# Performance work log

Hardware: AMD Instinct MI355X
Metric: run time of the kernel (lower is better)

## Reference

```python
import jax, jax.numpy as jnp
import numpy as np

N, K, D, H = 20000, 32, 256, 8
HD = D // H
DFF = 4 * D
EPS = 1e-5


def _layernorm(x, gamma, beta):
    mu = jnp.mean(x, axis=-1, keepdims=True)
    var = jnp.mean(jnp.square(x - mu), axis=-1, keepdims=True)
    return (x - mu) * jax.lax.rsqrt(var + EPS) * gamma + beta


def setup_inputs() -> dict:
    key = jax.random.key(0)
    ks = jax.random.split(key, 16)
    s = 0.02
    return {
        "x": jax.random.normal(ks[0], (N, D), jnp.float32),
        "attention_samples": jax.random.randint(ks[1], (N, K), 0, N),
        "Wq": jax.random.normal(ks[2], (D, D), jnp.float32) * s,
        "bq": jnp.zeros((D,), jnp.float32),
        "Wk": jax.random.normal(ks[3], (D, D), jnp.float32) * s,
        "bk": jnp.zeros((D,), jnp.float32),
        "Wv": jax.random.normal(ks[4], (D, D), jnp.float32) * s,
        "bv": jnp.zeros((D,), jnp.float32),
        "Wo": jax.random.normal(ks[5], (D, D), jnp.float32) * s,
        "bo": jnp.zeros((D,), jnp.float32),
        "W1": jax.random.normal(ks[6], (D, DFF), jnp.float32) * s,
        "b1": jnp.zeros((DFF,), jnp.float32),
        "W2": jax.random.normal(ks[7], (DFF, D), jnp.float32) * s,
        "b2": jnp.zeros((D,), jnp.float32),
        "g1": jnp.ones((D,), jnp.float32),
        "be1": jnp.zeros((D,), jnp.float32),
        "g2": jnp.ones((D,), jnp.float32),
        "be2": jnp.zeros((D,), jnp.float32),
    }


def reference(x, attention_samples, Wq, bq, Wk, bk, Wv, bv, Wo, bo,
              W1, b1, W2, b2, g1, be1, g2, be2):
    # --- per-node MHA: query = node itself, keys/values = k sampled neighbors ---
    q = (x @ Wq + bq).reshape(N, H, HD)                    # [N,H,hd]
    g = x[attention_samples]                               # [N,K,D] gathered neighbors
    kk = (g @ Wk + bk).reshape(N, K, H, HD)                # [N,K,H,hd]
    vv = (g @ Wv + bv).reshape(N, K, H, HD)
    scale = 1.0 / jnp.sqrt(jnp.asarray(HD, x.dtype))
    scores = jnp.einsum("nhd,nkhd->nhk", q, kk) * scale    # [N,H,K]
    attn = jax.nn.softmax(scores, axis=-1)
    o = jnp.einsum("nhk,nkhd->nhd", attn, vv).reshape(N, D)
    attn_out = o @ Wo + bo                                 # out_proj
    x = _layernorm(x + attn_out, g1, be1)
    # --- FFN ---
    ff = jax.nn.relu(x @ W1 + b1) @ W2 + b2
    x = _layernorm(x + ff, g2, be2)
    return x
```

## Files before the change

kernel.cpp:

```cpp
#include <hip/hip_runtime.h>

#define NN 20000
#define KNEI 32
#define DIM 256
#define NHEAD 8
#define HDIM 32
#define DFFN 1024
#define QKVD 768

typedef __attribute__((ext_vector_type(8))) __bf16 bf16x8;
typedef __attribute__((ext_vector_type(8))) unsigned short u16x8;
typedef __attribute__((ext_vector_type(4))) unsigned short u16x4;
typedef __attribute__((ext_vector_type(4))) float f32x4;
typedef __attribute__((ext_vector_type(2))) float f32x2;

static __device__ __forceinline__ float b2f(unsigned short u) {
    return __builtin_bit_cast(float, (unsigned)u << 16);
}
static __device__ __forceinline__ float blo(unsigned w) {
    return __builtin_bit_cast(float, w << 16);
}
static __device__ __forceinline__ float bhi(unsigned w) {
    return __builtin_bit_cast(float, w & 0xffff0000u);
}
static __device__ __forceinline__ unsigned short f2b(float f) {
    unsigned u = __builtin_bit_cast(unsigned, f);
    return (unsigned short)((u + 0x7fff + ((u >> 16) & 1)) >> 16);
}

static __device__ __forceinline__ unsigned char fp8enc(float v) {
#if defined(__HIP_DEVICE_COMPILE__) && __has_builtin(__builtin_amdgcn_cvt_pk_fp8_f32)
    return (unsigned char)(__builtin_amdgcn_cvt_pk_fp8_f32(v, v, 0u, false) & 0xffu);
#else
    unsigned u = __builtin_bit_cast(unsigned, v);
    unsigned s = u >> 31;
    unsigned a = u & 0x7fffffffu;
    if (a >= 0x43e00000u) return (unsigned char)((s << 7) | 0x7e);
    float af = __builtin_bit_cast(float, a);
    if (af < 0.015625f) {
        unsigned r = (unsigned)(af * 512.0f + 0.5f);
        if (r >= 8u) return (unsigned char)((s << 7) | 0x08);
        return (unsigned char)((s << 7) | r);
    }
    unsigned lsb = (a >> 20) & 1u;
    a += 0x7ffffu + lsb;
    unsigned e = (a >> 23) - 120u;
    unsigned m = (a >> 20) & 7u;
    unsigned code = (e << 3) | m;
    if (code > 0x7eu) code = 0x7eu;
    return (unsigned char)((s << 7) | code);
#endif
}

template<int SEL>
static __device__ __forceinline__ float fp8dec(unsigned word) {
#if defined(__HIP_DEVICE_COMPILE__) && __has_builtin(__builtin_amdgcn_cvt_f32_fp8)
    return __builtin_amdgcn_cvt_f32_fp8(word, SEL);
#else
    unsigned b = (word >> (SEL * 8)) & 0xffu;
    unsigned s = (b >> 7) & 1u;
    unsigned e = (b >> 3) & 0xfu;
    unsigned m = b & 7u;
    float v;
    if (e == 0) v = (float)m * 0.001953125f;
    else        v = __builtin_bit_cast(float, ((e + 120u) << 23) | (m << 20));
    return s ? -v : v;
#endif
}

template<bool HI>
static __device__ __forceinline__ f32x2 fp8pk(unsigned word) {
#if defined(__HIP_DEVICE_COMPILE__) && __has_builtin(__builtin_amdgcn_cvt_pk_f32_fp8)
    return __builtin_amdgcn_cvt_pk_f32_fp8((int)word, HI);
#else
    f32x2 r;
    r.x = fp8dec<HI ? 2 : 0>(word);
    r.y = fp8dec<HI ? 3 : 1>(word);
    return r;
#endif
}

#define GLD16(src, dst)                                                          \
    __builtin_amdgcn_global_load_lds(                                            \
        (const __attribute__((address_space(1))) void*)(const void*)(src),       \
        (__attribute__((address_space(3))) void*)(void*)(dst), 16, 0, 0)

template<int BM, int RELU, int WF32, int WBF16, int SPLIT>
__global__ __launch_bounds__(256) void gemm_mfma(const unsigned short* __restrict__ A,
                                                 const unsigned short* __restrict__ Bt,
                                                 const float* __restrict__ bias,
                                                 float* __restrict__ Cf,
                                                 unsigned short* __restrict__ Cb,
                                                 unsigned char* __restrict__ kvb,
                                                 int M, int N, int K)
{
    constexpr int BN = 128, BK = 32;
    constexpr int MI = BM / 32;
    constexpr int NI = BN / 32;

    __shared__ unsigned short As[BM * BK];
    __shared__ unsigned short Bs[BN * BK];

    const int tid  = threadIdx.x;
    const int wid  = tid >> 6;
    const int lane = tid & 63;
    const int bm = blockIdx.x * BM;
    const int bn = blockIdx.y * BN;
    const int wr = (wid >> 1) * (BM / 2);
    const int wc = (wid & 1) * (BN / 2);
    const int r0   = lane & 15;
    const int kblk = (lane >> 4) * 8;

    f32x4 acc[MI][NI];
    #pragma unroll
    for (int i = 0; i < MI; ++i)
        #pragma unroll
        for (int j = 0; j < NI; ++j)
            acc[i][j] = (f32x4){0.f, 0.f, 0.f, 0.f};

    for (int k0 = 0; k0 < K; k0 += BK) {
        constexpr int ACH = BM * 4;
        #pragma unroll
        for (int t = 0; t < ACH / 256; ++t) {
            int c = t * 256 + tid;
            int row = bm + (c >> 2);
            if (row >= M) row = M - 1;
            GLD16(A + (size_t)row * K + k0 + (c & 3) * 8,
                  &As[(t * 256 + wid * 64) * 8]);
        }
        #pragma unroll
        for (int t = 0; t < (BN * 4) / 256; ++t) {
            int c = t * 256 + tid;
            GLD16(Bt + (size_t)(bn + (c >> 2)) * K + k0 + (c & 3) * 8,
                  &Bs[(t * 256 + wid * 64) * 8]);
        }
        __syncthreads();

        bf16x8 af[MI], bfr[NI];
        #pragma unroll
        for (int mi = 0; mi < MI; ++mi)
            af[mi] = __builtin_bit_cast(bf16x8,
                     *(const u16x8*)&As[(wr + mi * 16 + r0) * BK + kblk]);
        #pragma unroll
        for (int ni = 0; ni < NI; ++ni)
            bfr[ni] = __builtin_bit_cast(bf16x8,
                     *(const u16x8*)&Bs[(wc + ni * 16 + r0) * BK + kblk]);
        #pragma unroll
        for (int mi = 0; mi < MI; ++mi)
            #pragma unroll
            for (int ni = 0; ni < NI; ++ni)
                acc[mi][ni] = __builtin_amdgcn_mfma_f32_16x16x32_bf16(
                    af[mi], bfr[ni], acc[mi][ni], 0, 0, 0);
        __syncthreads();
    }

    const int r4 = (lane >> 4) * 4;
    #pragma unroll
    for (int mi = 0; mi < MI; ++mi)
        #pragma unroll
        for (int ni = 0; ni < NI; ++ni) {
            const int col = bn + wc + ni * 16 + r0;
            const float bb = bias[col];
            #pragma unroll
            for (int r = 0; r < 4; ++r) {
                const int row = bm + wr + mi * 16 + r4 + r;
                if (row < M) {
                    float v = acc[mi][ni][r] + bb;
                    if (RELU) v = fmaxf(v, 0.f);
                    if (SPLIT) {
                        if (col < 256) Cb[(size_t)row * DIM + col] = f2b(v);
                        else kvb[(size_t)row * 512 + (col - 256)] = fp8enc(v);
                    } else {
                        if (WF32)  Cf[(size_t)row * N + col] = v;
                        if (WBF16) Cb[(size_t)row * N + col] = f2b(v);
                    }
                }
            }
        }
}

__global__ __launch_bounds__(256) void attn_f8(const unsigned short* __restrict__ q,
                                               const unsigned char* __restrict__ kv,
                                               const int* __restrict__ samp,
                                               unsigned short* __restrict__ o)
{
    const int n = blockIdx.x;
    const int tid = threadIdx.x;
    const int wid = tid >> 6;
    const int lane = tid & 63;
    const int j = lane & 31;
    const int hs = lane >> 5;
    const int h = wid * 2 + hs;

    const int kidx = samp[n * KNEI + j];

    const uint4* qp = (const uint4*)(q + (size_t)n * DIM + h * HDIM);
    const uint4 qa = qp[0], qb = qp[1], qc = qp[2], qd = qp[3];
    const unsigned qw[16] = {qa.x, qa.y, qa.z, qa.w, qb.x, qb.y, qb.z, qb.w,
                             qc.x, qc.y, qc.z, qc.w, qd.x, qd.y, qd.z, qd.w};

    const unsigned char* krow = kv + (size_t)kidx * 512 + h * HDIM;
    const uint4 k0 = *(const uint4*)krow;
    const uint4 k1 = *(const uint4*)(krow + 16);
    const unsigned kw[8] = {k0.x, k0.y, k0.z, k0.w, k1.x, k1.y, k1.z, k1.w};

    float s = 0.f;
    #pragma unroll
    for (int i = 0; i < 8; ++i) {
        f32x2 ka = fp8pk<false>(kw[i]);
        f32x2 kb = fp8pk<true>(kw[i]);
        unsigned q0 = qw[2 * i], q1 = qw[2 * i + 1];
        s = fmaf(blo(q0), ka.x, s);
        s = fmaf(bhi(q0), ka.y, s);
        s = fmaf(blo(q1), kb.x, s);
        s = fmaf(bhi(q1), kb.y, s);
    }
    s *= 0.17677669529663687f;

    float m = s;
    #pragma unroll
    for (int sh = 16; sh; sh >>= 1) m = fmaxf(m, __shfl_xor(m, sh));
    float e = __expf(s - m);
    float sum = e;
    #pragma unroll
    for (int sh = 16; sh; sh >>= 1) sum += __shfl_xor(sum, sh);
    const float p = __fdividef(e, sum);

    const int d = j;
    const int pbits = __builtin_bit_cast(int, p);
    const int pbase = hs * 128;
    const int voff = 256 + h * HDIM + d;
    float acc = 0.f;
    #pragma unroll
    for (int jj = 0; jj < KNEI; ++jj) {
        const int kj = __builtin_amdgcn_readlane(kidx, jj);
        const float pj = __builtin_bit_cast(float,
            __builtin_amdgcn_ds_bpermute(pbase + jj * 4, pbits));
        const unsigned char* vp = kv + (size_t)kj * 512 + voff;
        acc = fmaf(pj, fp8dec<0>((unsigned)*vp), acc);
    }
    o[(size_t)n * DIM + h * HDIM + d] = f2b(acc);
}

template<int XF32, int WFOUT>
__global__ __launch_bounds__(256) void add_ln(const float* __restrict__ xf,
                                              const unsigned short* __restrict__ xb,
                                              const unsigned short* __restrict__ y,
                                              const float* __restrict__ gamma,
                                              const float* __restrict__ beta,
                                              float* __restrict__ outf,
                                              unsigned short* __restrict__ outb, int M)
{
    const int row = blockIdx.x * 4 + (threadIdx.x >> 6);
    const int lane = threadIdx.x & 63;
    if (row >= M) return;

    float s0, s1, s2, s3;
    if (XF32) {
        const float4 xv = *(const float4*)(xf + (size_t)row * DIM + lane * 4);
        s0 = xv.x; s1 = xv.y; s2 = xv.z; s3 = xv.w;
    } else {
        const u16x4 xv = *(const u16x4*)(xb + (size_t)row * DIM + lane * 4);
        s0 = b2f(xv[0]); s1 = b2f(xv[1]); s2 = b2f(xv[2]); s3 = b2f(xv[3]);
    }
    const u16x4 yv = *(const u16x4*)(y + (size_t)row * DIM + lane * 4);
    s0 += b2f(yv[0]); s1 += b2f(yv[1]); s2 += b2f(yv[2]); s3 += b2f(yv[3]);

    float sum = s0 + s1 + s2 + s3;
    float sq = s0 * s0 + s1 * s1 + s2 * s2 + s3 * s3;
    #pragma unroll
    for (int sh = 32; sh; sh >>= 1) {
        sum += __shfl_xor(sum, sh);
        sq  += __shfl_xor(sq, sh);
    }
    float mean = sum * (1.f / 256.f);
    float var = sq * (1.f / 256.f) - mean * mean;
    float rstd = rsqrtf(var + 1e-5f);

    const float4 gv = *(const float4*)(gamma + lane * 4);
    const float4 bv = *(const float4*)(beta + lane * 4);
    float o0 = (s0 - mean) * rstd * gv.x + bv.x;
    float o1 = (s1 - mean) * rstd * gv.y + bv.y;
    float o2 = (s2 - mean) * rstd * gv.z + bv.z;
    float o3 = (s3 - mean) * rstd * gv.w + bv.w;
    if (WFOUT) {
        float4 ov = { o0, o1, o2, o3 };
        *(float4*)(outf + (size_t)row * DIM + lane * 4) = ov;
    } else {
        u16x4 bb = { f2b(o0), f2b(o1), f2b(o2), f2b(o3) };
        *(u16x4*)(outb + (size_t)row * DIM + lane * 4) = bb;
    }
}

__global__ __launch_bounds__(256) void cvt_bf16(const float* __restrict__ in,
                                                unsigned short* __restrict__ out, int n4)
{
    int i = blockIdx.x * 256 + threadIdx.x;
    if (i < n4) {
        float4 v = ((const float4*)in)[i];
        u16x4 b = { f2b(v.x), f2b(v.y), f2b(v.z), f2b(v.w) };
        ((u16x4*)out)[i] = b;
    }
}

__global__ __launch_bounds__(256) void cvt_transpose(const float* __restrict__ W,
                                                     unsigned short* __restrict__ Wt,
                                                     int K, int N)
{
    __shared__ float t[32][33];
    const int n0 = blockIdx.x * 32, k0 = blockIdx.y * 32;
    const int tx = threadIdx.x & 31, ty = threadIdx.x >> 5;
    #pragma unroll
    for (int i = 0; i < 32; i += 8)
        t[ty + i][tx] = W[(size_t)(k0 + ty + i) * N + n0 + tx];
    __syncthreads();
    #pragma unroll
    for (int i = 0; i < 32; i += 8)
        Wt[(size_t)(n0 + ty + i) * K + k0 + tx] = f2b(t[tx][ty + i]);
}

__global__ __launch_bounds__(256) void cvt_transpose4(const float* __restrict__ Wa,
                                                      const float* __restrict__ Wb,
                                                      const float* __restrict__ Wc,
                                                      const float* __restrict__ Wd,
                                                      unsigned short* __restrict__ Ta,
                                                      unsigned short* __restrict__ Tb,
                                                      unsigned short* __restrict__ Tc,
                                                      unsigned short* __restrict__ Td)
{
    const float* W; unsigned short* T;
    switch (blockIdx.z) {
        case 0:  W = Wa; T = Ta; break;
        case 1:  W = Wb; T = Tb; break;
        case 2:  W = Wc; T = Tc; break;
        default: W = Wd; T = Td; break;
    }
    __shared__ float t[32][33];
    const int n0 = blockIdx.x * 32, k0 = blockIdx.y * 32;
    const int tx = threadIdx.x & 31, ty = threadIdx.x >> 5;
    #pragma unroll
    for (int i = 0; i < 32; i += 8)
        t[ty + i][tx] = W[(size_t)(k0 + ty + i) * DIM + n0 + tx];
    __syncthreads();
    #pragma unroll
    for (int i = 0; i < 32; i += 8)
        T[(size_t)(n0 + ty + i) * DIM + k0 + tx] = f2b(t[tx][ty + i]);
}

__global__ void concat_bias(const float* a, const float* b, const float* c, float* out)
{
    int i = blockIdx.x * 256 + threadIdx.x;
    if (i < 256) out[i] = a[i];
    else if (i < 512) out[i] = b[i - 256];
    else if (i < 768) out[i] = c[i - 512];
}

extern "C" void kernel_launch(void* const* d_in, const int* in_sizes, int n_in,
                              void* d_out, int out_size, void* d_ws, size_t ws_size,
                              hipStream_t stream)
{
    const float* x    = (const float*)d_in[0];
    const int*   samp = (const int*)  d_in[1];
    const float* Wq = (const float*)d_in[2];  const float* bq = (const float*)d_in[3];
    const float* Wk = (const float*)d_in[4];  const float* bk = (const float*)d_in[5];
    const float* Wv = (const float*)d_in[6];  const float* bv = (const float*)d_in[7];
    const float* Wo = (const float*)d_in[8];  const float* bo = (const float*)d_in[9];
    const float* W1 = (const float*)d_in[10]; const float* b1 = (const float*)d_in[11];
    const float* W2 = (const float*)d_in[12]; const float* b2 = (const float*)d_in[13];
    const float* g1 = (const float*)d_in[14]; const float* be1 = (const float*)d_in[15];
    const float* g2 = (const float*)d_in[16]; const float* be2 = (const float*)d_in[17];
    float* out = (float*)d_out;

    char* w = (char*)d_ws;
    const size_t MB = 1u << 20;
    unsigned short* WqkvT = (unsigned short*)(w + 0);
    unsigned short* WoT   = (unsigned short*)(w + 393216);
    unsigned short* W1T   = (unsigned short*)(w + 524288);
    unsigned short* W2T   = (unsigned short*)(w + 1048576);
    float*          bqkv  = (float*)(w + 1572864);
    unsigned short* xb    = (unsigned short*)(w + 2 * MB);
    unsigned short* qb    = (unsigned short*)(w + 13 * MB);
    unsigned char*  kvb   = (unsigned char*) (w + 24 * MB);
    unsigned short* ob    = xb;
    unsigned short* attno = (unsigned short*)(w + 35 * MB);
    unsigned short* x1b   = (unsigned short*)(w + 46 * MB);
    unsigned short* hmid  = (unsigned short*)(w + 57 * MB);
    unsigned short* ffb   = attno;

    const dim3 blk(256);

    cvt_transpose4<<<dim3(8, 8, 4), blk, 0, stream>>>(
        Wq, Wk, Wv, Wo, WqkvT, WqkvT + 256 * 256, WqkvT + 512 * 256, WoT);
    cvt_transpose<<<dim3(32, 8), blk, 0, stream>>>(W1, W1T, DIM, DFFN);
    cvt_transpose<<<dim3(8, 32), blk, 0, stream>>>(W2, W2T, DFFN, DIM);
    concat_bias<<<dim3(3), blk, 0, stream>>>(bq, bk, bv, bqkv);
    cvt_bf16<<<dim3((NN * DIM / 4 + 255) / 256), blk, 0, stream>>>(x, xb, NN * DIM / 4);

    gemm_mfma<128, 0, 0, 0, 1><<<dim3(157, 6), blk, 0, stream>>>(
        xb, WqkvT, bqkv, nullptr, qb, kvb, NN, QKVD, DIM);

    attn_f8<<<dim3(NN), blk, 0, stream>>>(qb, kvb, samp, ob);

    gemm_mfma<64, 0, 0, 1, 0><<<dim3(313, 2), blk, 0, stream>>>(
        ob, WoT, bo, nullptr, attno, nullptr, NN, DIM, DIM);
    add_ln<1, 0><<<dim3(NN / 4), blk, 0, stream>>>(x, nullptr, attno, g1, be1,
                                                   nullptr, x1b, NN);

    gemm_mfma<128, 1, 0, 1, 0><<<dim3(157, 8), blk, 0, stream>>>(
        x1b, W1T, b1, nullptr, hmid, nullptr, NN, DFFN, DIM);
    gemm_mfma<64, 0, 0, 1, 0><<<dim3(313, 2), blk, 0, stream>>>(
        hmid, W2T, b2, nullptr, ffb, nullptr, NN, DIM, DFFN);
    add_ln<0, 1><<<dim3(NN / 4), blk, 0, stream>>>(nullptr, x1b, ffb, g2, be2,
                                                   out, nullptr, NN);
}
```

Measured before the change: 188.9 us.

## Double-buffer GEMM LDS tiles and process two nodes per attention block

The MFMA GEMM now keeps two LDS buffers and issues the global-to-LDS loads for the next K tile before computing on the current one, dropping one barrier per iteration so load latency overlaps with MFMA work. The attention kernel packs two nodes into each 512-thread block, halving the grid size. The cost is doubled LDS per GEMM block, which may lower occupancy. Correctness relies on the async LDS loads for the next tile having completed by the single trailing barrier.

```diff
diff --git a/kernel.cpp b/kernel.cpp
--- a/kernel.cpp
+++ b/kernel.cpp
@@ -98,8 +98,8 @@
     constexpr int MI = BM / 32;
     constexpr int NI = BN / 32;
 
-    __shared__ unsigned short As[BM * BK];
-    __shared__ unsigned short Bs[BN * BK];
+    __shared__ unsigned short As[2][BM * BK];
+    __shared__ unsigned short Bs[2][BN * BK];
 
     const int tid  = threadIdx.x;
     const int wid  = tid >> 6;
@@ -111,47 +111,58 @@
     const int r0   = lane & 15;
     const int kblk = (lane >> 4) * 8;
 
-    f32x4 acc[MI][NI];
-    #pragma unroll
-    for (int i = 0; i < MI; ++i)
-        #pragma unroll
-        for (int j = 0; j < NI; ++j)
-            acc[i][j] = (f32x4){0.f, 0.f, 0.f, 0.f};
-
-    for (int k0 = 0; k0 < K; k0 += BK) {
-        constexpr int ACH = BM * 4;
-        #pragma unroll
-        for (int t = 0; t < ACH / 256; ++t) {
-            int c = t * 256 + tid;
-            int row = bm + (c >> 2);
+    int arow = bm + (tid >> 2);
+    const int aoff = (tid & 3) * 8;
+
+    auto stage = [&](int buf, int k0) {
+        #pragma unroll
+        for (int t = 0; t < (BM * 4) / 256; ++t) {
+            int row = bm + ((t * 256 + tid) >> 2);
             if (row >= M) row = M - 1;
-            GLD16(A + (size_t)row * K + k0 + (c & 3) * 8,
-                  &As[(t * 256 + wid * 64) * 8]);
+            GLD16(A + (size_t)row * K + k0 + aoff,
+                  &As[buf][(t * 256 + wid * 64) * 8]);
         }
         #pragma unroll
         for (int t = 0; t < (BN * 4) / 256; ++t) {
             int c = t * 256 + tid;
             GLD16(Bt + (size_t)(bn + (c >> 2)) * K + k0 + (c & 3) * 8,
-                  &Bs[(t * 256 + wid * 64) * 8]);
+                  &Bs[buf][(t * 256 + wid * 64) * 8]);
         }
-        __syncthreads();
+    };
+    (void)arow;
+
+    f32x4 acc[MI][NI];
+    #pragma unroll
+    for (int i = 0; i < MI; ++i)
+        #pragma unroll
+        for (int j = 0; j < NI; ++j)
+            acc[i][j] = (f32x4){0.f, 0.f, 0.f, 0.f};
+
+    stage(0, 0);
+    __syncthreads();
+
+    int cur = 0;
+    for (int k0 = 0; k0 < K; k0 += BK) {
+        if (k0 + BK < K) stage(cur ^ 1, k0 + BK);
 
         bf16x8 af[MI], bfr[NI];
         #pragma unroll
         for (int mi = 0; mi < MI; ++mi)
             af[mi] = __builtin_bit_cast(bf16x8,
-                     *(const u16x8*)&As[(wr + mi * 16 + r0) * BK + kblk]);
+                     *(const u16x8*)&As[cur][(wr + mi * 16 + r0) * BK + kblk]);
         #pragma unroll
         for (int ni = 0; ni < NI; ++ni)
             bfr[ni] = __builtin_bit_cast(bf16x8,
-                     *(const u16x8*)&Bs[(wc + ni * 16 + r0) * BK + kblk]);
+                     *(const u16x8*)&Bs[cur][(wc + ni * 16 + r0) * BK + kblk]);
         #pragma unroll
         for (int mi = 0; mi < MI; ++mi)
             #pragma unroll
             for (int ni = 0; ni < NI; ++ni)
                 acc[mi][ni] = __builtin_amdgcn_mfma_f32_16x16x32_bf16(
                     af[mi], bfr[ni], acc[mi][ni], 0, 0, 0);
+
         __syncthreads();
+        cur ^= 1;
     }
 
     const int r4 = (lane >> 4) * 4;
@@ -179,13 +190,13 @@
         }
 }
 
-__global__ __launch_bounds__(256) void attn_f8(const unsigned short* __restrict__ q,
+__global__ __launch_bounds__(512) void attn_f8(const unsigned short* __restrict__ q,
                                                const unsigned char* __restrict__ kv,
                                                const int* __restrict__ samp,
                                                unsigned short* __restrict__ o)
 {
-    const int n = blockIdx.x;
-    const int tid = threadIdx.x;
+    const int n = blockIdx.x * 2 + (threadIdx.x >> 8);
+    const int tid = threadIdx.x & 255;
     const int wid = tid >> 6;
     const int lane = tid & 63;
     const int j = lane & 31;
@@ -399,7 +410,7 @@
     gemm_mfma<128, 0, 0, 0, 1><<<dim3(157, 6), blk, 0, stream>>>(
         xb, WqkvT, bqkv, nullptr, qb, kvb, NN, QKVD, DIM);
 
-    attn_f8<<<dim3(NN), blk, 0, stream>>>(qb, kvb, samp, ob);
+    attn_f8<<<dim3(NN / 2), dim3(512), 0, stream>>>(qb, kvb, samp, ob);
 
     gemm_mfma<64, 0, 0, 1, 0><<<dim3(313, 2), blk, 0, stream>>>(
         ob, WoT, bo, nullptr, attno, nullptr, NN, DIM, DIM);
```

After: 188.9 us. About the same (+0.0%).

## Store fp8 K/V head-major and group attention blocks by head pair

Applied to the files above, without the earlier changes.

The QKV GEMM epilogue now writes fp8 K and V into a head-major layout, [head][node][64] with K and V interleaved per head, instead of row-major 512-byte rows. The attention kernel is remapped so each block handles one head pair across four nodes rather than all heads of one node. Each head's K/V table (about 1.28 MB) is then compact, and blocks processed together touch the same head's data, which is meant to improve cache locality for the random neighbor gathers. The cost is scattered fp8 stores in the GEMM epilogue and a different q/o access pattern.

```diff
diff --git a/kernel.cpp b/kernel.cpp
--- a/kernel.cpp
+++ b/kernel.cpp
@@ -91,7 +91,7 @@
                                                  const float* __restrict__ bias,
                                                  float* __restrict__ Cf,
                                                  unsigned short* __restrict__ Cb,
-                                                 unsigned char* __restrict__ kvb,
+                                                 unsigned char* __restrict__ kvh,
                                                  int M, int N, int K)
 {
     constexpr int BN = 128, BK = 32;
@@ -119,9 +119,8 @@
             acc[i][j] = (f32x4){0.f, 0.f, 0.f, 0.f};
 
     for (int k0 = 0; k0 < K; k0 += BK) {
-        constexpr int ACH = BM * 4;
-        #pragma unroll
-        for (int t = 0; t < ACH / 256; ++t) {
+        #pragma unroll
+        for (int t = 0; t < (BM * 4) / 256; ++t) {
             int c = t * 256 + tid;
             int row = bm + (c >> 2);
             if (row >= M) row = M - 1;
@@ -168,8 +167,15 @@
                     float v = acc[mi][ni][r] + bb;
                     if (RELU) v = fmaxf(v, 0.f);
                     if (SPLIT) {
-                        if (col < 256) Cb[(size_t)row * DIM + col] = f2b(v);
-                        else kvb[(size_t)row * 512 + (col - 256)] = fp8enc(v);
+                        if (col < 256) {
+                            Cb[(size_t)row * DIM + col] = f2b(v);
+                        } else {
+                            const int cc  = col - 256;
+                            const int isV = cc >> 8;
+                            const int hh  = (cc & 255) >> 5;
+                            const int dd  = cc & 31;
+                            kvh[((size_t)hh * NN + row) * 64 + isV * 32 + dd] = fp8enc(v);
+                        }
                     } else {
                         if (WF32)  Cf[(size_t)row * N + col] = v;
                         if (WBF16) Cb[(size_t)row * N + col] = f2b(v);
@@ -180,17 +186,19 @@
 }
 
 __global__ __launch_bounds__(256) void attn_f8(const unsigned short* __restrict__ q,
-                                               const unsigned char* __restrict__ kv,
+                                               const unsigned char* __restrict__ kvh,
                                                const int* __restrict__ samp,
                                                unsigned short* __restrict__ o)
 {
-    const int n = blockIdx.x;
+    const int bid = blockIdx.x;
+    const int hp  = bid & 3;
     const int tid = threadIdx.x;
     const int wid = tid >> 6;
+    const int n   = (bid >> 2) * 4 + wid;
     const int lane = tid & 63;
     const int j = lane & 31;
     const int hs = lane >> 5;
-    const int h = wid * 2 + hs;
+    const int h = hp * 2 + hs;
 
     const int kidx = samp[n * KNEI + j];
 
@@ -199,7 +207,7 @@
     const unsigned qw[16] = {qa.x, qa.y, qa.z, qa.w, qb.x, qb.y, qb.z, qb.w,
                              qc.x, qc.y, qc.z, qc.w, qd.x, qd.y, qd.z, qd.w};
 
-    const unsigned char* krow = kv + (size_t)kidx * 512 + h * HDIM;
+    const unsigned char* krow = kvh + ((size_t)h * NN + kidx) * 64;
     const uint4 k0 = *(const uint4*)krow;
     const uint4 k1 = *(const uint4*)(krow + 16);
     const unsigned kw[8] = {k0.x, k0.y, k0.z, k0.w, k1.x, k1.y, k1.z, k1.w};
@@ -229,15 +237,14 @@
     const int d = j;
     const int pbits = __builtin_bit_cast(int, p);
     const int pbase = hs * 128;
-    const int voff = 256 + h * HDIM + d;
+    const unsigned vbase = (unsigned)((size_t)h * NN * 64) + 32 + d;
     float acc = 0.f;
     #pragma unroll
     for (int jj = 0; jj < KNEI; ++jj) {
         const int kj = __builtin_amdgcn_readlane(kidx, jj);
         const float pj = __builtin_bit_cast(float,
             __builtin_amdgcn_ds_bpermute(pbase + jj * 4, pbits));
-        const unsigned char* vp = kv + (size_t)kj * 512 + voff;
-        acc = fmaf(pj, fp8dec<0>((unsigned)*vp), acc);
+        acc = fmaf(pj, fp8dec<0>((unsigned)kvh[vbase + (unsigned)kj * 64u]), acc);
     }
     o[(size_t)n * DIM + h * HDIM + d] = f2b(acc);
 }
@@ -380,7 +387,7 @@
     float*          bqkv  = (float*)(w + 1572864);
     unsigned short* xb    = (unsigned short*)(w + 2 * MB);
     unsigned short* qb    = (unsigned short*)(w + 13 * MB);
-    unsigned char*  kvb   = (unsigned char*) (w + 24 * MB);
+    unsigned char*  kvh   = (unsigned char*) (w + 24 * MB);
     unsigned short* ob    = xb;
     unsigned short* attno = (unsigned short*)(w + 35 * MB);
     unsigned short* x1b   = (unsigned short*)(w + 46 * MB);
@@ -397,9 +404,9 @@
     cvt_bf16<<<dim3((NN * DIM / 4 + 255) / 256), blk, 0, stream>>>(x, xb, NN * DIM / 4);
 
     gemm_mfma<128, 0, 0, 0, 1><<<dim3(157, 6), blk, 0, stream>>>(
-        xb, WqkvT, bqkv, nullptr, qb, kvb, NN, QKVD, DIM);
-
-    attn_f8<<<dim3(NN), blk, 0, stream>>>(qb, kvb, samp, ob);
+        xb, WqkvT, bqkv, nullptr, qb, kvh, NN, QKVD, DIM);
+
+    attn_f8<<<dim3(NN), blk, 0, stream>>>(qb, kvh, samp, ob);
 
     gemm_mfma<64, 0, 0, 1, 0><<<dim3(313, 2), blk, 0, stream>>>(
         ob, WoT, bo, nullptr, attno, nullptr, NN, DIM, DIM);
```

New measurement: 196.3 us. +3.9%, slower.
